# Optimization experiments

Measured on AMD Instinct MI355X. Metric: run time of the kernel, lower is better.

Reference implementation:

```python
import jax, jax.numpy as jnp
import numpy as np

DIM = 512
HEADS = 8
HEAD_DIM = DIM // HEADS
MLP = 2048
EPS = 1e-5


def _layer_norm(x, g, b):
    mu = jnp.mean(x, axis=-1, keepdims=True)
    var = jnp.var(x, axis=-1, keepdims=True)
    return (x - mu) * jax.lax.rsqrt(var + EPS) * g + b


def setup_inputs() -> dict:
    key = jax.random.key(0)
    ks = jax.random.split(key, 12)
    s = 1.0 / np.sqrt(DIM)
    sm = 1.0 / np.sqrt(MLP)
    return {
        "x": jax.random.normal(ks[0], (2, 4096, DIM), dtype=jnp.float32),
        "Wq": jax.random.normal(ks[1], (DIM, DIM), dtype=jnp.float32) * s,
        "Wk": jax.random.normal(ks[2], (DIM, DIM), dtype=jnp.float32) * s,
        "Wv": jax.random.normal(ks[3], (DIM, DIM), dtype=jnp.float32) * s,
        "Wo": jax.random.normal(ks[4], (DIM, DIM), dtype=jnp.float32) * s,
        "bo": jnp.zeros((DIM,), dtype=jnp.float32),
        "W1": jax.random.normal(ks[5], (DIM, MLP), dtype=jnp.float32) * s,
        "b1": jnp.zeros((MLP,), dtype=jnp.float32),
        "W2": jax.random.normal(ks[6], (MLP, DIM), dtype=jnp.float32) * sm,
        "b2": jnp.zeros((DIM,), dtype=jnp.float32),
        "g1": jnp.ones((DIM,), dtype=jnp.float32),
        "be1": jnp.zeros((DIM,), dtype=jnp.float32),
        "g2": jnp.ones((DIM,), dtype=jnp.float32),
        "be2": jnp.zeros((DIM,), dtype=jnp.float32),
    }


def reference(x, Wq, Wk, Wv, Wo, bo, W1, b1, W2, b2, g1, be1, g2, be2):
    b, n, d = x.shape
    # --- pre-norm multi-head attention ---
    h = _layer_norm(x, g1, be1)
    q = (h @ Wq).reshape(b, n, HEADS, HEAD_DIM).transpose(0, 2, 1, 3)  # [b,h,n,hd]
    k = (h @ Wk).reshape(b, n, HEADS, HEAD_DIM).transpose(0, 2, 1, 3)
    v = (h @ Wv).reshape(b, n, HEADS, HEAD_DIM).transpose(0, 2, 1, 3)
    scores = jnp.einsum("bhqd,bhkd->bhqk", q, k) / np.sqrt(HEAD_DIM)  # [b,h,n,n]
    attn = jax.nn.softmax(scores, axis=-1)
    out = jnp.einsum("bhqk,bhkd->bhqd", attn, v)
    out = out.transpose(0, 2, 1, 3).reshape(b, n, d)
    x = x + out @ Wo + bo
    # --- pre-norm feed-forward ---
    h2 = _layer_norm(x, g2, be2)
    ff = jax.nn.gelu(h2 @ W1 + b1, approximate=False) @ W2 + b2
    return x + ff
```

## Files before the change

kernel.cpp:

```cpp
#include <hip/hip_runtime.h>
#include <math.h>

#define BB   2
#define SEQ  4096
#define DIM  512
#define NH   8
#define HD   64
#define MLPD 2048
#define ROWS (BB*SEQ)
#define SZ   (ROWS*DIM)
#define EPSV 1e-5f

typedef __attribute__((ext_vector_type(8))) short bf16x8;
typedef __attribute__((ext_vector_type(4))) float f32x4;

#if __has_builtin(__builtin_amdgcn_exp2f)
#define EXP2(x) __builtin_amdgcn_exp2f(x)
#else
#define EXP2(x) exp2f(x)
#endif

__device__ __forceinline__ ushort f2bf(float f) {
    unsigned u = __float_as_uint(f);
    u += 0x7fffu + ((u >> 16) & 1u);
    return (ushort)(u >> 16);
}
__device__ __forceinline__ unsigned pack2bf(float a, float b) {
    return (unsigned)f2bf(a) | ((unsigned)f2bf(b) << 16);
}
__device__ __forceinline__ unsigned pack2bf_tr(float a, float b) {
    return (__float_as_uint(a) >> 16) | (__float_as_uint(b) & 0xffff0000u);
}

__device__ __forceinline__ void gload16(const ushort* g, ushort* l) {
    __builtin_amdgcn_global_load_lds(
        (const __attribute__((address_space(1))) unsigned*)g,
        (__attribute__((address_space(3))) unsigned*)l, 16, 0, 0);
}

__global__ __launch_bounds__(128) void ln_kernel(const float* __restrict__ x,
        const float* __restrict__ g, const float* __restrict__ be,
        ushort* __restrict__ out)
{
    int row = blockIdx.x;
    int tid = threadIdx.x;
    const float4 v = ((const float4*)(x + (size_t)row*DIM))[tid];
    float s  = v.x + v.y + v.z + v.w;
    float ss = v.x*v.x + v.y*v.y + v.z*v.z + v.w*v.w;
    #pragma unroll
    for (int off = 32; off > 0; off >>= 1) {
        s  += __shfl_down(s,  off);
        ss += __shfl_down(ss, off);
    }
    __shared__ float red[4];
    if ((tid & 63) == 0) { red[(tid>>6)*2+0] = s; red[(tid>>6)*2+1] = ss; }
    __syncthreads();
    float sum = red[0] + red[2], sumsq = red[1] + red[3];
    float mu  = sum * (1.0f/DIM);
    float var = sumsq * (1.0f/DIM) - mu*mu;
    float rs  = rsqrtf(var + EPSV);
    float4 gv = ((const float4*)g)[tid];
    float4 bv = ((const float4*)be)[tid];
    ushort4 o;
    o.x = f2bf((v.x - mu)*rs*gv.x + bv.x);
    o.y = f2bf((v.y - mu)*rs*gv.y + bv.y);
    o.z = f2bf((v.z - mu)*rs*gv.z + bv.z);
    o.w = f2bf((v.w - mu)*rs*gv.w + bv.w);
    ((ushort4*)(out + (size_t)row*DIM))[tid] = o;
}

__global__ __launch_bounds__(256) void wtrans_kernel(const float* __restrict__ W,
        ushort* __restrict__ Wt, int K, int N)
{
    __shared__ ushort T[64][65];
    int n0 = blockIdx.x*64, k0 = blockIdx.y*64;
    int tid = threadIdx.x;
    #pragma unroll
    for (int p = 0; p < 4; ++p) {
        int r = p*16 + (tid>>4), c = (tid&15)<<2;
        float4 w4 = *(const float4*)(W + (size_t)(k0+r)*N + n0 + c);
        T[c+0][r] = f2bf(w4.x); T[c+1][r] = f2bf(w4.y);
        T[c+2][r] = f2bf(w4.z); T[c+3][r] = f2bf(w4.w);
    }
    __syncthreads();
    #pragma unroll
    for (int p = 0; p < 4; ++p) {
        int n = p*16 + (tid>>4), k = (tid&15)<<2;
        ushort4 o; o.x = T[n][k]; o.y = T[n][k+1]; o.z = T[n][k+2]; o.w = T[n][k+3];
        *(ushort4*)(Wt + (size_t)(n0+n)*K + k0 + k) = o;
    }
}

__global__ __launch_bounds__(256) void wtrans4_kernel(
        const float* __restrict__ W0, const float* __restrict__ W1,
        const float* __restrict__ W2, const float* __restrict__ W3,
        ushort* __restrict__ Wt)
{
    __shared__ ushort T[64][65];
    int z = blockIdx.z;
    const float* W = (z==0) ? W0 : (z==1) ? W1 : (z==2) ? W2 : W3;
    ushort* Wtz = Wt + (size_t)z*512*512;
    int n0 = blockIdx.x*64, k0 = blockIdx.y*64;
    int tid = threadIdx.x;
    #pragma unroll
    for (int p = 0; p < 4; ++p) {
        int r = p*16 + (tid>>4), c = (tid&15)<<2;
        float4 w4 = *(const float4*)(W + (size_t)(k0+r)*512 + n0 + c);
        T[c+0][r] = f2bf(w4.x); T[c+1][r] = f2bf(w4.y);
        T[c+2][r] = f2bf(w4.z); T[c+3][r] = f2bf(w4.w);
    }
    __syncthreads();
    #pragma unroll
    for (int p = 0; p < 4; ++p) {
        int n = p*16 + (tid>>4), k = (tid&15)<<2;
        ushort4 o; o.x = T[n][k]; o.y = T[n][k+1]; o.z = T[n][k+2]; o.w = T[n][k+3];
        *(ushort4*)(Wtz + (size_t)(n0+n)*512 + k0 + k) = o;
    }
}

template<int BM, int NT>
__global__ __launch_bounds__(NT) void gemm_bf16_kernel(
        const ushort* __restrict__ A,
        const ushort* __restrict__ Wta, const ushort* __restrict__ Wtb, const ushort* __restrict__ Wtc,
        const float* __restrict__ bias, const float* __restrict__ resid,
        void* __restrict__ outv, int M, int Nn, int K, int flags)
{
    constexpr int AISS = (BM*4)/NT;
    constexpr int BISS = 256/NT;
    __shared__ ushort As[2][BM*32];
    __shared__ ushort Bs[2][64*32];
    int tid = threadIdx.x;
    int w = tid >> 6, lane = tid & 63, quad = lane >> 4, col = lane & 15;

    int nx = gridDim.x;
    int nwg = nx * gridDim.y;
    int flat = blockIdx.x + nx * blockIdx.y;
    int bx, by;
    if ((nwg & 7) == 0) {
        int cpx = nwg >> 3;
        int slot = (flat & 7) * cpx + (flat >> 3);
        bx = slot % nx; by = slot / nx;
    } else { bx = blockIdx.x; by = blockIdx.y; }
    int row0 = by * BM, col0 = bx * 64;
    int wm0 = w * 32;

    const ushort* Wt; int wcol0, ostride, obase_col;
    float qscale = 1.0f;
    float* outF = nullptr; ushort* outB = nullptr;
    if (flags & 1) {
        int sel = col0 >> 9;
        Wt = (sel == 0) ? Wta : ((sel == 1) ? Wtb : Wtc);
        wcol0 = col0 & 511; ostride = 512; obase_col = wcol0;
        outB = (ushort*)outv + (size_t)sel * ((size_t)M * 512);
        if (sel == 0) qscale = 0.125f * 1.44269504088896f;
        flags |= 16;
    } else {
        Wt = Wta; wcol0 = col0; ostride = Nn; obase_col = col0;
        if (flags & 16) outB = (ushort*)outv; else outF = (float*)outv;
    }

    f32x4 acc[2][4];
    #pragma unroll
    for (int i = 0; i < 2; ++i)
        #pragma unroll
        for (int j = 0; j < 4; ++j) acc[i][j] = (f32x4){0.f,0.f,0.f,0.f};

    const ushort* Ag = A  + (size_t)(row0  + (tid >> 2))*K + ((tid & 3) << 3);
    const ushort* Bg = Wt + (size_t)(wcol0 + (tid >> 2))*K + ((tid & 3) << 3);

    auto issue = [&](ushort* Ad, ushort* Bd, int ko) {
        #pragma unroll
        for (int it = 0; it < AISS; ++it)
            gload16(Ag + ko + (size_t)(it*(NT/4))*K, Ad + it*NT*8 + tid*8);
        #pragma unroll
        for (int it = 0; it < BISS; ++it)
            gload16(Bg + ko + (size_t)(it*(NT/4))*K, Bd + it*NT*8 + tid*8);
    };
    auto compute = [&](const ushort* Ab, const ushort* Bb) {
        bf16x8 af[2], bfr[4];
        #pragma unroll
        for (int i = 0; i < 2; ++i)
            af[i] = *(const bf16x8*)(Ab + (wm0 + i*16 + col)*32 + quad*8);
        #pragma unroll
        for (int j = 0; j < 4; ++j)
            bfr[j] = *(const bf16x8*)(Bb + (j*16 + col)*32 + quad*8);
        #pragma unroll
        for (int i = 0; i < 2; ++i)
            #pragma unroll
            for (int j = 0; j < 4; ++j)
                acc[i][j] = __builtin_amdgcn_mfma_f32_16x16x32_bf16(af[i], bfr[j], acc[i][j], 0, 0, 0);
    };

    int niter = K >> 5;
    issue(As[0], Bs[0], 0);
    for (int i = 0; i < niter; i += 2) {
        __syncthreads();
        if (i + 1 < niter) issue(As[1], Bs[1], (i+1)*32);
        compute(As[0], Bs[0]);
        __syncthreads();
        if (i + 2 < niter) issue(As[0], Bs[0], (i+2)*32);
        compute(As[1], Bs[1]);
    }

    #pragma unroll
    for (int i = 0; i < 2; ++i) {
        #pragma unroll
        for (int r = 0; r < 4; ++r) {
            int row = row0 + wm0 + i*16 + quad*4 + r;
            #pragma unroll
            for (int j = 0; j < 4; ++j) {
                int oc = obase_col + j*16 + col;
                float o = acc[i][j][r] * qscale;
                if (flags & 8) o += bias[oc];
                if (flags & 2) o = 0.5f*o*(1.f + erff(o*0.70710678118654752f));
                if (flags & 4) o += resid[(size_t)row*ostride + oc];
                if (flags & 16) outB[(size_t)row*ostride + oc] = f2bf(o);
                else            outF[(size_t)row*ostride + oc] = o;
            }
        }
    }
}

__global__ __launch_bounds__(256) void vtrans_kernel(const ushort* __restrict__ v,
                                                     ushort* __restrict__ vt)
{
    int tt = blockIdx.x, bh = blockIdx.y;
    int b = bh >> 3, h = bh & 7;
    int tid = threadIdx.x;
    int d = tid >> 2, t0 = (tid & 3) << 4;
    ushort tmp[16];
    #pragma unroll
    for (int i = 0; i < 16; ++i) {
        int kp = t0 + i;
        int korig = ((kp>>5)*2 + ((kp>>2)&1))*16 + ((kp>>3)&3)*4 + (kp&3);
        tmp[i] = v[(size_t)(b*SEQ + tt*64 + korig)*DIM + h*HD + d];
    }
    unsigned u[8];
    #pragma unroll
    for (int j = 0; j < 8; ++j) u[j] = (unsigned)tmp[2*j] | ((unsigned)tmp[2*j+1] << 16);
    ushort* dst = vt + ((size_t)bh*HD + d)*SEQ + tt*64 + t0;
    *(uint4*)(dst)     = make_uint4(u[0],u[1],u[2],u[3]);
    *(uint4*)(dst + 8) = make_uint4(u[4],u[5],u[6],u[7]);
}

__global__ __launch_bounds__(256, 2) void attn_mfma_kernel(
        const ushort* __restrict__ q, const ushort* __restrict__ k,
        const ushort* __restrict__ vt, ushort* __restrict__ out)
{
    __shared__ __align__(16) ushort Kt[2][64][72];
    __shared__ __align__(16) ushort Vt[2][64][72];

    int flat = blockIdx.x + (blockIdx.y << 5);
    int xcd  = flat & 7, slot = flat >> 3;
    int bh   = (xcd << 1) | (slot >> 5);
    int qt   = slot & 31;
    int b = bh >> 3, h = bh & 7;
    int tid = threadIdx.x;
    int w = tid >> 6, lane = tid & 63;
    int quad = lane >> 4, col = lane & 15;
    int qw = w >> 1, kw = w & 1;
    int qn0 = qt*128 + qw*64;
    int krow0 = kw << 5;

    bf16x8 aq[4][2];
    #pragma unroll
    for (int mt = 0; mt < 4; ++mt) {
        const ushort* qp = q + (size_t)(b*SEQ + qn0 + mt*16 + col)*DIM + h*HD + quad*8;
        aq[mt][0] = *(const bf16x8*)(qp);
        aq[mt][1] = *(const bf16x8*)(qp + 32);
    }
    const short one_bf = (short)0x3F80;
    const bf16x8 ones = {one_bf,one_bf,one_bf,one_bf,one_bf,one_bf,one_bf,one_bf};
    const f32x4 zf = {0.f,0.f,0.f,0.f};

    f32x4 ot[4][4];
    f32x4 ol[4];
    #pragma unroll
    for (int mt = 0; mt < 4; ++mt) {
        ol[mt] = zf;
        #pragma unroll
        for (int t4 = 0; t4 < 4; ++t4) ot[mt][t4] = zf;
    }

    int skey = tid >> 2, sd0 = (tid & 3) << 4;
    bf16x8 kr[2], vr[2];
    auto load_tile = [&](int t) {
        const ushort* kp = k + (size_t)(b*SEQ + t*64 + skey)*DIM + h*HD + sd0;
        kr[0] = *(const bf16x8*)(kp);
        kr[1] = *(const bf16x8*)(kp + 8);
        const ushort* vp = vt + ((size_t)bh*HD + skey)*SEQ + t*64 + sd0;
        vr[0] = *(const bf16x8*)(vp);
        vr[1] = *(const bf16x8*)(vp + 8);
    };
    auto store_tile = [&](int p) {
        *(bf16x8*)&Kt[p][skey][sd0]     = kr[0];
        *(bf16x8*)&Kt[p][skey][sd0+8]   = kr[1];
        *(bf16x8*)&Vt[p][skey][sd0]     = vr[0];
        *(bf16x8*)&Vt[p][skey][sd0+8]   = vr[1];
    };

    load_tile(0);
    store_tile(0);
    __syncthreads();

    for (int t = 0; t < SEQ/64; ++t) {
        int p = t & 1;
        if (t + 1 < SEQ/64) load_tile(t + 1);

        bf16x8 kf0[2], kf1[2], vf[4];
        #pragma unroll
        for (int kb = 0; kb < 2; ++kb) {
            const ushort* kbp = &Kt[p][krow0 + kb*16 + col][quad*8];
            kf0[kb] = *(const bf16x8*)(kbp);
            kf1[kb] = *(const bf16x8*)(kbp + 32);
        }
        #pragma unroll
        for (int t4 = 0; t4 < 4; ++t4)
            vf[t4] = *(const bf16x8*)&Vt[p][t4*16 + col][krow0 + quad*8];

        f32x4 sc[4][2];
        __builtin_amdgcn_s_setprio(1);
        #pragma unroll
        for (int mt = 0; mt < 4; ++mt)
            #pragma unroll
            for (int kb = 0; kb < 2; ++kb) {
                sc[mt][kb] = __builtin_amdgcn_mfma_f32_16x16x32_bf16(kf0[kb], aq[mt][0], zf, 0, 0, 0);
                sc[mt][kb] = __builtin_amdgcn_mfma_f32_16x16x32_bf16(kf1[kb], aq[mt][1], sc[mt][kb], 0, 0, 0);
            }
        __builtin_amdgcn_s_setprio(0);

        union PU { bf16x8 v; uint4 u; };
        PU pb[4];
        #pragma unroll
        for (int mt = 0; mt < 4; ++mt) {
            pb[mt].u.x = pack2bf_tr(EXP2(sc[mt][0][0]), EXP2(sc[mt][0][1]));
            pb[mt].u.y = pack2bf_tr(EXP2(sc[mt][0][2]), EXP2(sc[mt][0][3]));
            pb[mt].u.z = pack2bf_tr(EXP2(sc[mt][1][0]), EXP2(sc[mt][1][1]));
            pb[mt].u.w = pack2bf_tr(EXP2(sc[mt][1][2]), EXP2(sc[mt][1][3]));
        }

        __builtin_amdgcn_s_setprio(1);
        #pragma unroll
        for (int mt = 0; mt < 4; ++mt) {
            #pragma unroll
            for (int t4 = 0; t4 < 4; ++t4)
                ot[mt][t4] = __builtin_amdgcn_mfma_f32_16x16x32_bf16(vf[t4], pb[mt].v, ot[mt][t4], 0, 0, 0);
            ol[mt] = __builtin_amdgcn_mfma_f32_16x16x32_bf16(ones, pb[mt].v, ol[mt], 0, 0, 0);
        }
        __builtin_amdgcn_s_setprio(0);

        if (t + 1 < SEQ/64) store_tile(p ^ 1);
        __syncthreads();
    }

    f32x4* redA = (f32x4*)Kt;
    f32x4* redB = (f32x4*)Vt;
    int rbase = ((qw << 6) + lane) * 9;
    if (kw) {
        #pragma unroll
        for (int t4 = 0; t4 < 4; ++t4) {
            redA[rbase + t4]     = ot[0][t4];
            redA[rbase + 4 + t4] = ot[1][t4];
            redB[rbase + t4]     = ot[2][t4];
            redB[rbase + 4 + t4] = ot[3][t4];
        }
        redA[rbase + 8] = (f32x4){ol[0][0], ol[1][0], ol[2][0], ol[3][0]};
    }
    __syncthreads();
    if (!kw) {
        f32x4 olp = redA[rbase + 8];
        #pragma unroll
        for (int mt = 0; mt < 4; ++mt) {
            float inv = 1.0f / (ol[mt][0] + olp[mt]);
            #pragma unroll
            for (int t4 = 0; t4 < 4; ++t4) {
                f32x4 r = (mt < 2) ? redA[rbase + mt*4 + t4]
                                   : redB[rbase + (mt-2)*4 + t4];
                f32x4 o = ot[mt][t4] + r;
                ushort4 o4;
                o4.x = f2bf(o[0] * inv);
                o4.y = f2bf(o[1] * inv);
                o4.z = f2bf(o[2] * inv);
                o4.w = f2bf(o[3] * inv);
                *(ushort4*)(out + (size_t)(b*SEQ + qn0 + mt*16 + col)*DIM + h*HD + t4*16 + quad*4) = o4;
            }
        }
    }
}

extern "C" void kernel_launch(void* const* d_in, const int* in_sizes, int n_in,
                              void* d_out, int out_size, void* d_ws, size_t ws_size,
                              hipStream_t stream)
{
    (void)in_sizes; (void)n_in; (void)out_size; (void)ws_size;
    const float* x   = (const float*)d_in[0];
    const float* Wq  = (const float*)d_in[1];
    const float* Wk  = (const float*)d_in[2];
    const float* Wv  = (const float*)d_in[3];
    const float* Wo  = (const float*)d_in[4];
    const float* bo  = (const float*)d_in[5];
    const float* W1  = (const float*)d_in[6];
    const float* b1  = (const float*)d_in[7];
    const float* W2  = (const float*)d_in[8];
    const float* b2  = (const float*)d_in[9];
    const float* g1  = (const float*)d_in[10];
    const float* be1 = (const float*)d_in[11];
    const float* g2  = (const float*)d_in[12];
    const float* be2 = (const float*)d_in[13];

    ushort* u = (ushort*)d_ws;
    float*  x2    = (float*)u;
    ushort* h     = u + 2*(size_t)SZ;
    ushort* qb    = u + 3*(size_t)SZ;
    ushort* kb    = u + 4*(size_t)SZ;
    ushort* vb    = u + 5*(size_t)SZ;
    ushort* vtb   = u + 6*(size_t)SZ;
    ushort* attnb = u + 7*(size_t)SZ;
    ushort* ff1   = u + 3*(size_t)SZ;
    ushort* wqkv  = u + 8*(size_t)SZ;
    ushort* wto   = wqkv + 3*(size_t)512*512;
    ushort* wt1   = wqkv + 4*(size_t)512*512;
    ushort* wt2   = wt1  + (size_t)512*2048;
    float*  outp  = (float*)d_out;

    wtrans4_kernel<<<dim3(8,8,4), 256, 0, stream>>>(Wq, Wk, Wv, Wo, wqkv);
    wtrans_kernel<<<dim3(32,8), 256, 0, stream>>>(W1, wt1, 512, 2048);
    wtrans_kernel<<<dim3(8,32), 256, 0, stream>>>(W2, wt2, 2048, 512);

    ln_kernel<<<ROWS, 128, 0, stream>>>(x, g1, be1, h);
    gemm_bf16_kernel<128,256><<<dim3(1536/64, ROWS/128), 256, 0, stream>>>(
        h, wqkv, wqkv + (size_t)512*512, wqkv + 2*(size_t)512*512,
        nullptr, nullptr, qb, ROWS, 1536, DIM, 1);
    vtrans_kernel<<<dim3(SEQ/64, BB*NH), 256, 0, stream>>>(vb, vtb);
    attn_mfma_kernel<<<dim3(SEQ/128, BB*NH), 256, 0, stream>>>(qb, kb, vtb, attnb);
    gemm_bf16_kernel<64,128><<<dim3(DIM/64, ROWS/64), 128, 0, stream>>>(
        attnb, wto, wto, wto, bo, x, x2, ROWS, DIM, DIM, 8|4);
    ln_kernel<<<ROWS, 128, 0, stream>>>(x2, g2, be2, h);
    gemm_bf16_kernel<128,256><<<dim3(MLPD/64, ROWS/128), 256, 0, stream>>>(
        h, wt1, wt1, wt1, b1, nullptr, ff1, ROWS, MLPD, DIM, 8|2|16);
    gemm_bf16_kernel<64,128><<<dim3(DIM/64, ROWS/64), 128, 0, stream>>>(
        ff1, wt2, wt2, wt2, b2, x2, outp, ROWS, DIM, MLPD, 8|4);
}
```

Baseline: 337.9 us.

## Add 128x128-tile bf16 MFMA GEMM kernel for QKV, FF1 and FF2 projections

Introduces a new GEMM kernel with 128x128 output tiles per 256-thread block, where each wave computes a 64x64 sub-tile of 4x4 MFMA fragments. It uses double-buffered LDS loads via global_load_lds and XCD-aware block remapping. The kernel replaces the 128x64 and 64x64 tiled GEMMs for the QKV, MLP-up and MLP-down projections to raise operand reuse per loaded tile. In exchange, the blocks have higher register pressure and the grids are smaller: the down-projection launches only 256 blocks, which may underfill the GPU.

```diff
diff --git a/kernel.cpp b/kernel.cpp
--- a/kernel.cpp
+++ b/kernel.cpp
@@ -24,9 +24,6 @@
     unsigned u = __float_as_uint(f);
     u += 0x7fffu + ((u >> 16) & 1u);
     return (ushort)(u >> 16);
-}
-__device__ __forceinline__ unsigned pack2bf(float a, float b) {
-    return (unsigned)f2bf(a) | ((unsigned)f2bf(b) << 16);
 }
 __device__ __forceinline__ unsigned pack2bf_tr(float a, float b) {
     return (__float_as_uint(a) >> 16) | (__float_as_uint(b) & 0xffff0000u);
@@ -115,6 +112,106 @@
         int n = p*16 + (tid>>4), k = (tid&15)<<2;
         ushort4 o; o.x = T[n][k]; o.y = T[n][k+1]; o.z = T[n][k+2]; o.w = T[n][k+3];
         *(ushort4*)(Wtz + (size_t)(n0+n)*512 + k0 + k) = o;
+    }
+}
+
+__global__ __launch_bounds__(256) void gemm128_kernel(
+        const ushort* __restrict__ A,
+        const ushort* __restrict__ Wta, const ushort* __restrict__ Wtb, const ushort* __restrict__ Wtc,
+        const float* __restrict__ bias, const float* __restrict__ resid,
+        void* __restrict__ outv, int M, int Nn, int K, int flags)
+{
+    __shared__ ushort As[2][128*32];
+    __shared__ ushort Bs[2][128*32];
+    int tid = threadIdx.x;
+    int w = tid >> 6, lane = tid & 63, quad = lane >> 4, col = lane & 15;
+    int wr = w >> 1, wc = w & 1;
+
+    int nx = gridDim.x;
+    int nwg = nx * gridDim.y;
+    int flat = blockIdx.x + nx * blockIdx.y;
+    int bx, by;
+    if ((nwg & 7) == 0) {
+        int cpx = nwg >> 3;
+        int slot = (flat & 7) * cpx + (flat >> 3);
+        bx = slot % nx; by = slot / nx;
+    } else { bx = blockIdx.x; by = blockIdx.y; }
+    int row0 = by * 128, col0 = bx * 128;
+
+    const ushort* Wt; int wcol0, ostride, obase_col;
+    float qscale = 1.0f;
+    float* outF = nullptr; ushort* outB = nullptr;
+    if (flags & 1) {
+        int sel = col0 >> 9;
+        Wt = (sel == 0) ? Wta : ((sel == 1) ? Wtb : Wtc);
+        wcol0 = col0 & 511; ostride = 512; obase_col = wcol0;
+        outB = (ushort*)outv + (size_t)sel * ((size_t)M * 512);
+        if (sel == 0) qscale = 0.125f * 1.44269504088896f;
+        flags |= 16;
+    } else {
+        Wt = Wta; wcol0 = col0; ostride = Nn; obase_col = col0;
+        if (flags & 16) outB = (ushort*)outv; else outF = (float*)outv;
+    }
+
+    f32x4 acc[4][4];
+    #pragma unroll
+    for (int i = 0; i < 4; ++i)
+        #pragma unroll
+        for (int j = 0; j < 4; ++j) acc[i][j] = (f32x4){0.f,0.f,0.f,0.f};
+
+    const ushort* Ag = A  + (size_t)(row0  + (tid >> 2))*K + ((tid & 3) << 3);
+    const ushort* Bg = Wt + (size_t)(wcol0 + (tid >> 2))*K + ((tid & 3) << 3);
+
+    auto issue = [&](ushort* Ad, ushort* Bd, int ko) {
+        #pragma unroll
+        for (int it = 0; it < 2; ++it)
+            gload16(Ag + ko + (size_t)(it*64)*K, Ad + it*2048 + tid*8);
+        #pragma unroll
+        for (int it = 0; it < 2; ++it)
+            gload16(Bg + ko + (size_t)(it*64)*K, Bd + it*2048 + tid*8);
+    };
+    auto compute = [&](const ushort* Ab, const ushort* Bb) {
+        bf16x8 af[4], bfr[4];
+        #pragma unroll
+        for (int i = 0; i < 4; ++i)
+            af[i] = *(const bf16x8*)(Ab + (wr*64 + i*16 + col)*32 + quad*8);
+        #pragma unroll
+        for (int j = 0; j < 4; ++j)
+            bfr[j] = *(const bf16x8*)(Bb + (wc*64 + j*16 + col)*32 + quad*8);
+        #pragma unroll
+        for (int i = 0; i < 4; ++i)
+            #pragma unroll
+            for (int j = 0; j < 4; ++j)
+                acc[i][j] = __builtin_amdgcn_mfma_f32_16x16x32_bf16(af[i], bfr[j], acc[i][j], 0, 0, 0);
+    };
+
+    int niter = K >> 5;
+    issue(As[0], Bs[0], 0);
+    for (int i = 0; i < niter; i += 2) {
+        __syncthreads();
+        if (i + 1 < niter) issue(As[1], Bs[1], (i+1)*32);
+        compute(As[0], Bs[0]);
+        __syncthreads();
+        if (i + 2 < niter) issue(As[0], Bs[0], (i+2)*32);
+        compute(As[1], Bs[1]);
+    }
+
+    #pragma unroll
+    for (int i = 0; i < 4; ++i) {
+        #pragma unroll
+        for (int r = 0; r < 4; ++r) {
+            int row = row0 + wr*64 + i*16 + quad*4 + r;
+            #pragma unroll
+            for (int j = 0; j < 4; ++j) {
+                int oc = obase_col + wc*64 + j*16 + col;
+                float o = acc[i][j][r] * qscale;
+                if (flags & 8) o += bias[oc];
+                if (flags & 2) o = 0.5f*o*(1.f + erff(o*0.70710678118654752f));
+                if (flags & 4) o += resid[(size_t)row*ostride + oc];
+                if (flags & 16) outB[(size_t)row*ostride + oc] = f2bf(o);
+                else            outF[(size_t)row*ostride + oc] = o;
+            }
+        }
     }
 }
 
@@ -428,7 +525,7 @@
     wtrans_kernel<<<dim3(8,32), 256, 0, stream>>>(W2, wt2, 2048, 512);
 
     ln_kernel<<<ROWS, 128, 0, stream>>>(x, g1, be1, h);
-    gemm_bf16_kernel<128,256><<<dim3(1536/64, ROWS/128), 256, 0, stream>>>(
+    gemm128_kernel<<<dim3(1536/128, ROWS/128), 256, 0, stream>>>(
         h, wqkv, wqkv + (size_t)512*512, wqkv + 2*(size_t)512*512,
         nullptr, nullptr, qb, ROWS, 1536, DIM, 1);
     vtrans_kernel<<<dim3(SEQ/64, BB*NH), 256, 0, stream>>>(vb, vtb);
@@ -436,8 +533,8 @@
     gemm_bf16_kernel<64,128><<<dim3(DIM/64, ROWS/64), 128, 0, stream>>>(
         attnb, wto, wto, wto, bo, x, x2, ROWS, DIM, DIM, 8|4);
     ln_kernel<<<ROWS, 128, 0, stream>>>(x2, g2, be2, h);
-    gemm_bf16_kernel<128,256><<<dim3(MLPD/64, ROWS/128), 256, 0, stream>>>(
+    gemm128_kernel<<<dim3(MLPD/128, ROWS/128), 256, 0, stream>>>(
         h, wt1, wt1, wt1, b1, nullptr, ff1, ROWS, MLPD, DIM, 8|2|16);
-    gemm_bf16_kernel<64,128><<<dim3(DIM/64, ROWS/64), 128, 0, stream>>>(
+    gemm128_kernel<<<dim3(DIM/128, ROWS/128), 256, 0, stream>>>(
         ff1, wt2, wt2, wt2, b2, x2, outp, ROWS, DIM, MLPD, 8|4);
 }
```

After: 362.4 us. +7.2%, slower.

## Stream K/V tiles per wave via direct global-to-LDS loads, drop block barriers

Applied to the files above, without the earlier changes.

Each wave now loads only its own half of the K/V tile into private, double-buffered LDS slices using global_load_lds. The K slice uses an XOR-swizzled layout. Loads are waited on with s_waitcnt vmcnt instead of a __syncthreads per tile, so the register staging and the block-wide barrier in the main loop go away. In exchange, the two q-waves sharing a key half each load the same K/V data, which doubles global/L2 traffic. Correctness also relies on the vmcnt accounting and on each wave touching only its own buffers.

```diff
diff --git a/kernel.cpp b/kernel.cpp
--- a/kernel.cpp
+++ b/kernel.cpp
@@ -24,9 +24,6 @@
     unsigned u = __float_as_uint(f);
     u += 0x7fffu + ((u >> 16) & 1u);
     return (ushort)(u >> 16);
-}
-__device__ __forceinline__ unsigned pack2bf(float a, float b) {
-    return (unsigned)f2bf(a) | ((unsigned)f2bf(b) << 16);
 }
 __device__ __forceinline__ unsigned pack2bf_tr(float a, float b) {
     return (__float_as_uint(a) >> 16) | (__float_as_uint(b) & 0xffff0000u);
@@ -247,8 +244,8 @@
         const ushort* __restrict__ q, const ushort* __restrict__ k,
         const ushort* __restrict__ vt, ushort* __restrict__ out)
 {
-    __shared__ __align__(16) ushort Kt[2][64][72];
-    __shared__ __align__(16) ushort Vt[2][64][72];
+    __shared__ __align__(16) ushort KB[4][2][2048];
+    __shared__ __align__(16) ushort VB[4][2][2048];
 
     int flat = blockIdx.x + (blockIdx.y << 5);
     int xcd  = flat & 7, slot = flat >> 3;
@@ -261,6 +258,26 @@
     int qw = w >> 1, kw = w & 1;
     int qn0 = qt*128 + qw*64;
     int krow0 = kw << 5;
+    int c7 = col & 7;
+
+    const ushort* kgp = k + (size_t)(b*SEQ + krow0 + (lane>>3))*DIM + h*HD
+                          + (((lane&7) ^ (lane>>3)) << 3);
+    const ushort* vgp = vt + ((size_t)bh*HD + (lane>>2))*SEQ + krow0 + ((lane&3)<<3);
+
+    auto issueKV = [&](int buf, const ushort* kg, const ushort* vg) {
+        ushort* kd = KB[w][buf] + lane*8;
+        gload16(kg,                    kd);
+        gload16(kg + (size_t) 8*DIM,   kd + 512);
+        gload16(kg + (size_t)16*DIM,   kd + 1024);
+        gload16(kg + (size_t)24*DIM,   kd + 1536);
+        ushort* vd = VB[w][buf] + lane*8;
+        gload16(vg,                    vd);
+        gload16(vg + (size_t)16*SEQ,   vd + 512);
+        gload16(vg + (size_t)32*SEQ,   vd + 1024);
+        gload16(vg + (size_t)48*SEQ,   vd + 1536);
+    };
+
+    issueKV(0, kgp, vgp);
 
     bf16x8 aq[4][2];
     #pragma unroll
@@ -282,41 +299,19 @@
         for (int t4 = 0; t4 < 4; ++t4) ot[mt][t4] = zf;
     }
 
-    int skey = tid >> 2, sd0 = (tid & 3) << 4;
-    bf16x8 kr[2], vr[2];
-    auto load_tile = [&](int t) {
-        const ushort* kp = k + (size_t)(b*SEQ + t*64 + skey)*DIM + h*HD + sd0;
-        kr[0] = *(const bf16x8*)(kp);
-        kr[1] = *(const bf16x8*)(kp + 8);
-        const ushort* vp = vt + ((size_t)bh*HD + skey)*SEQ + t*64 + sd0;
-        vr[0] = *(const bf16x8*)(vp);
-        vr[1] = *(const bf16x8*)(vp + 8);
-    };
-    auto store_tile = [&](int p) {
-        *(bf16x8*)&Kt[p][skey][sd0]     = kr[0];
-        *(bf16x8*)&Kt[p][skey][sd0+8]   = kr[1];
-        *(bf16x8*)&Vt[p][skey][sd0]     = vr[0];
-        *(bf16x8*)&Vt[p][skey][sd0+8]   = vr[1];
-    };
-
-    load_tile(0);
-    store_tile(0);
-    __syncthreads();
-
-    for (int t = 0; t < SEQ/64; ++t) {
-        int p = t & 1;
-        if (t + 1 < SEQ/64) load_tile(t + 1);
-
+    auto compute_tile = [&](int p) {
+        const ushort* KBb = KB[w][p];
+        const ushort* VBb = VB[w][p];
         bf16x8 kf0[2], kf1[2], vf[4];
         #pragma unroll
         for (int kb = 0; kb < 2; ++kb) {
-            const ushort* kbp = &Kt[p][krow0 + kb*16 + col][quad*8];
-            kf0[kb] = *(const bf16x8*)(kbp);
-            kf1[kb] = *(const bf16x8*)(kbp + 32);
+            const ushort* rp = KBb + (kb*16 + col)*64;
+            kf0[kb] = *(const bf16x8*)(rp + (((quad    ) ^ c7) << 3));
+            kf1[kb] = *(const bf16x8*)(rp + (((quad + 4) ^ c7) << 3));
         }
         #pragma unroll
         for (int t4 = 0; t4 < 4; ++t4)
-            vf[t4] = *(const bf16x8*)&Vt[p][t4*16 + col][krow0 + quad*8];
+            vf[t4] = *(const bf16x8*)(VBb + (t4*16 + col)*32 + quad*8);
 
         f32x4 sc[4][2];
         __builtin_amdgcn_s_setprio(1);
@@ -348,13 +343,20 @@
             ol[mt] = __builtin_amdgcn_mfma_f32_16x16x32_bf16(ones, pb[mt].v, ol[mt], 0, 0, 0);
         }
         __builtin_amdgcn_s_setprio(0);
-
-        if (t + 1 < SEQ/64) store_tile(p ^ 1);
-        __syncthreads();
-    }
-
-    f32x4* redA = (f32x4*)Kt;
-    f32x4* redB = (f32x4*)Vt;
+    };
+
+    for (int t = 0; t < SEQ/64 - 1; ++t) {
+        kgp += (size_t)64*DIM; vgp += 64;
+        issueKV((t & 1) ^ 1, kgp, vgp);
+        asm volatile("s_waitcnt vmcnt(8)" ::: "memory");
+        compute_tile(t & 1);
+    }
+    asm volatile("s_waitcnt vmcnt(0)" ::: "memory");
+    compute_tile((SEQ/64 - 1) & 1);
+
+    __syncthreads();
+    f32x4* redA = (f32x4*)KB;
+    f32x4* redB = (f32x4*)VB;
     int rbase = ((qw << 6) + lane) * 9;
     if (kw) {
         #pragma unroll
```

Result: no change. 340.9 us (+0.9%).

## Split attention across two key halves and combine partials in a separate kernel

Applied to the files above, without the earlier changes.

The attention kernel now splits the key sequence into two halves, doubling the grid from 512 to 1024 blocks. Each block writes unnormalised fp32 partial outputs and per-row softmax sums into reused workspace buffers. A new combine kernel adds the two partials, normalises, and writes bf16 for the output projection. The aim is more parallelism and occupancy (launch bounds raised to 4 blocks per SM), in exchange for extra fp32 global traffic and one more kernel launch. Because scores are exponentiated without a max subtraction, adding the partials this way is algebraically valid.

```diff
diff --git a/kernel.cpp b/kernel.cpp
--- a/kernel.cpp
+++ b/kernel.cpp
@@ -25,8 +25,8 @@
     u += 0x7fffu + ((u >> 16) & 1u);
     return (ushort)(u >> 16);
 }
-__device__ __forceinline__ unsigned pack2bf(float a, float b) {
-    return (unsigned)f2bf(a) | ((unsigned)f2bf(b) << 16);
+__device__ __forceinline__ float b2f(ushort u) {
+    return __uint_as_float(((unsigned)u) << 16);
 }
 __device__ __forceinline__ unsigned pack2bf_tr(float a, float b) {
     return (__float_as_uint(a) >> 16) | (__float_as_uint(b) & 0xffff0000u);
@@ -243,17 +243,23 @@
     *(uint4*)(dst + 8) = make_uint4(u[4],u[5],u[6],u[7]);
 }
 
-__global__ __launch_bounds__(256, 2) void attn_mfma_kernel(
+__global__ __launch_bounds__(256, 4) void attn_mfma_kernel(
         const ushort* __restrict__ q, const ushort* __restrict__ k,
-        const ushort* __restrict__ vt, ushort* __restrict__ out)
+        const ushort* __restrict__ vt,
+        float* __restrict__ p0,
+        float* __restrict__ p1lo,
+        float* __restrict__ p1hi,
+        float* __restrict__ lbuf)
 {
     __shared__ __align__(16) ushort Kt[2][64][72];
     __shared__ __align__(16) ushort Vt[2][64][72];
 
-    int flat = blockIdx.x + (blockIdx.y << 5);
+    int flat = blockIdx.x + (blockIdx.y << 6);
     int xcd  = flat & 7, slot = flat >> 3;
-    int bh   = (xcd << 1) | (slot >> 5);
-    int qt   = slot & 31;
+    int bh   = (xcd << 1) | (slot >> 6);
+    int rem  = slot & 63;
+    int qt   = rem >> 1;
+    int ks   = rem & 1;
     int b = bh >> 3, h = bh & 7;
     int tid = threadIdx.x;
     int w = tid >> 6, lane = tid & 63;
@@ -261,6 +267,7 @@
     int qw = w >> 1, kw = w & 1;
     int qn0 = qt*128 + qw*64;
     int krow0 = kw << 5;
+    int t0 = ks * (SEQ/128);
 
     bf16x8 aq[4][2];
     #pragma unroll
@@ -299,13 +306,13 @@
         *(bf16x8*)&Vt[p][skey][sd0+8]   = vr[1];
     };
 
-    load_tile(0);
+    load_tile(t0);
     store_tile(0);
     __syncthreads();
 
-    for (int t = 0; t < SEQ/64; ++t) {
-        int p = t & 1;
-        if (t + 1 < SEQ/64) load_tile(t + 1);
+    for (int tt = 0; tt < SEQ/128; ++tt) {
+        int p = tt & 1;
+        if (tt + 1 < SEQ/128) load_tile(t0 + tt + 1);
 
         bf16x8 kf0[2], kf1[2], vf[4];
         #pragma unroll
@@ -349,7 +356,7 @@
         }
         __builtin_amdgcn_s_setprio(0);
 
-        if (t + 1 < SEQ/64) store_tile(p ^ 1);
+        if (tt + 1 < SEQ/128) store_tile(p ^ 1);
         __syncthreads();
     }
 
@@ -368,24 +375,44 @@
     }
     __syncthreads();
     if (!kw) {
+        float* pbase = (ks == 0) ? p0 : ((b == 0) ? p1lo : (p1hi - (size_t)SEQ*DIM));
         f32x4 olp = redA[rbase + 8];
         #pragma unroll
         for (int mt = 0; mt < 4; ++mt) {
-            float inv = 1.0f / (ol[mt][0] + olp[mt]);
+            float lsum = ol[mt][0] + olp[mt];
+            if (lane < 16)
+                lbuf[(size_t)ks*ROWS*NH + (size_t)(b*SEQ + qn0 + mt*16 + lane)*NH + h] = lsum;
             #pragma unroll
             for (int t4 = 0; t4 < 4; ++t4) {
                 f32x4 r = (mt < 2) ? redA[rbase + mt*4 + t4]
                                    : redB[rbase + (mt-2)*4 + t4];
                 f32x4 o = ot[mt][t4] + r;
-                ushort4 o4;
-                o4.x = f2bf(o[0] * inv);
-                o4.y = f2bf(o[1] * inv);
-                o4.z = f2bf(o[2] * inv);
-                o4.w = f2bf(o[3] * inv);
-                *(ushort4*)(out + (size_t)(b*SEQ + qn0 + mt*16 + col)*DIM + h*HD + t4*16 + quad*4) = o4;
+                *(f32x4*)(pbase + (size_t)(b*SEQ + qn0 + mt*16 + col)*DIM
+                          + h*HD + t4*16 + quad*4) = o;
             }
         }
     }
+}
+
+__global__ __launch_bounds__(128) void attn_combine_kernel(
+        const float* __restrict__ p0, const float* __restrict__ p1lo,
+        const float* __restrict__ p1hi, const float* __restrict__ lbuf,
+        ushort* __restrict__ out)
+{
+    int row = blockIdx.x, tid = threadIdx.x;
+    const float* p1 = (row < SEQ) ? p1lo + (size_t)row*DIM
+                                  : p1hi + (size_t)(row - SEQ)*DIM;
+    int h = tid >> 4;
+    float l = lbuf[(size_t)row*NH + h] + lbuf[(size_t)ROWS*NH + (size_t)row*NH + h];
+    float inv = 1.0f / l;
+    float4 a = ((const float4*)(p0 + (size_t)row*DIM))[tid];
+    float4 c = ((const float4*)p1)[tid];
+    ushort4 o;
+    o.x = f2bf((a.x + c.x) * inv);
+    o.y = f2bf((a.y + c.y) * inv);
+    o.z = f2bf((a.z + c.z) * inv);
+    o.w = f2bf((a.w + c.w) * inv);
+    ((ushort4*)(out + (size_t)row*DIM))[tid] = o;
 }
 
 extern "C" void kernel_launch(void* const* d_in, const int* in_sizes, int n_in,
@@ -423,6 +450,12 @@
     ushort* wt2   = wt1  + (size_t)512*2048;
     float*  outp  = (float*)d_out;
 
+    float* part0 = x2;
+    float* p1lo  = (float*)vb;
+    float* p1hi  = (float*)attnb;
+    float* lbuf  = (float*)h;
+    ushort* aout = qb;
+
     wtrans4_kernel<<<dim3(8,8,4), 256, 0, stream>>>(Wq, Wk, Wv, Wo, wqkv);
     wtrans_kernel<<<dim3(32,8), 256, 0, stream>>>(W1, wt1, 512, 2048);
     wtrans_kernel<<<dim3(8,32), 256, 0, stream>>>(W2, wt2, 2048, 512);
@@ -432,9 +465,11 @@
         h, wqkv, wqkv + (size_t)512*512, wqkv + 2*(size_t)512*512,
         nullptr, nullptr, qb, ROWS, 1536, DIM, 1);
     vtrans_kernel<<<dim3(SEQ/64, BB*NH), 256, 0, stream>>>(vb, vtb);
-    attn_mfma_kernel<<<dim3(SEQ/128, BB*NH), 256, 0, stream>>>(qb, kb, vtb, attnb);
+    attn_mfma_kernel<<<dim3(64, 16), 256, 0, stream>>>(qb, kb, vtb,
+        part0, p1lo, p1hi, lbuf);
+    attn_combine_kernel<<<ROWS, 128, 0, stream>>>(part0, p1lo, p1hi, lbuf, aout);
     gemm_bf16_kernel<64,128><<<dim3(DIM/64, ROWS/64), 128, 0, stream>>>(
-        attnb, wto, wto, wto, bo, x, x2, ROWS, DIM, DIM, 8|4);
+        aout, wto, wto, wto, bo, x, x2, ROWS, DIM, DIM, 8|4);
     ln_kernel<<<ROWS, 128, 0, stream>>>(x2, g2, be2, h);
     gemm_bf16_kernel<128,256><<<dim3(MLPD/64, ROWS/128), 256, 0, stream>>>(
         h, wt1, wt1, wt1, b1, nullptr, ff1, ROWS, MLPD, DIM, 8|2|16);
```

Result: slower. 822.9 us (+143.5%).
